# Kernel tuning notes

Hardware: AMD Instinct MI355X
Metric: run time of the kernel (lower is better)

Reference implementation:

```python
import jax, jax.numpy as jnp
import numpy as np

B, S, IN, OUT, R, E = 8, 2048, 4096, 4096, 16, 64
ALPHA = 1.0


def setup_inputs() -> dict:
    ks = jax.random.split(jax.random.key(0), 7)
    return {
        "x": jax.random.normal(ks[0], (B, S, IN), jnp.float32),
        "query_signal": jax.random.normal(ks[1], (B, IN), jnp.float32),
        "A_pool": jax.random.normal(ks[2], (E, R, IN), jnp.float32),
        # original inits B pool to zeros; use small random values for a non-degenerate baseline
        "B_pool": jax.random.normal(ks[3], (E, OUT, R), jnp.float32) * 0.02,
        "W_rA": jax.random.normal(ks[4], (E, IN), jnp.float32) * 0.02,
        "b_rA": jnp.zeros((E,), jnp.float32),
        "W_rB": jax.random.normal(ks[5], (E, IN), jnp.float32) * 0.02,
        "b_rB": jnp.zeros((E,), jnp.float32),
        "cfs_W": jax.random.normal(ks[6], (R, IN, E), jnp.float32),
    }


def reference(x, query_signal, A_pool, B_pool, W_rA, b_rA, W_rB, b_rB, cfs_W):
    ranks = jnp.arange(R)  # rank slot k pairs with the k-th top-k expert index
    # IFS router A -> top-r expert indices per sample
    g_A_scores = query_signal @ W_rA.T + b_rA            # (B, E)
    _, idx_A = jax.lax.top_k(g_A_scores, R)              # (B, R)
    # gather: k-th selected expert contributes its k-th rank row
    lora_A = A_pool[idx_A, ranks[None, :], :]            # (B, R, IN)
    # router B scores: IFS linear + CFS content score (detached lora_A)
    g_B_scores = (query_signal @ W_rB.T + b_rB
                  + jnp.einsum('bri,rie->be', jax.lax.stop_gradient(lora_A), cfs_W))  # (B, E)
    _, idx_B = jax.lax.top_k(g_B_scores, R)              # (B, R)
    lora_B = jnp.transpose(B_pool, (0, 2, 1))[idx_B, ranks[None, :], :]  # (B, R, OUT)
    # two batched low-rank matmuls
    after_A = jnp.einsum('bsi,bri->bsr', x, lora_A)      # (B, S, R)
    lora_delta = jnp.einsum('bsr,bro->bso', after_A, lora_B)  # (B, S, OUT)
    return lora_delta * ALPHA
```

## Files before the change

### kernel.cpp

```cpp
#include <hip/hip_runtime.h>

#define B_ 8
#define S_ 2048
#define IN_ 4096
#define OUT_ 4096
#define R_ 16
#define E_ 64

typedef float v4f __attribute__((ext_vector_type(4)));

__device__ __forceinline__ float4 ntload4(const float* p) {
  v4f t = __builtin_nontemporal_load((const v4f*)p);
  float4 r; r.x = t.x; r.y = t.y; r.z = t.z; r.w = t.w; return r;
}
__device__ __forceinline__ void ntstore4(float* p, float4 v) {
  v4f t; t.x = v.x; t.y = v.y; t.z = v.z; t.w = v.w;
  __builtin_nontemporal_store(t, (v4f*)p);
}

__device__ __forceinline__ float dot4(float4 a, float4 b) {
  return a.x*b.x + a.y*b.y + a.z*b.z + a.w*b.w;
}

__device__ __forceinline__ void topk16(float v, int* __restrict__ dst) {
  const int lane = threadIdx.x & 63;
  for (int r = 0; r < R_; ++r) {
    float mv = v; int mi = lane;
    #pragma unroll
    for (int off = 1; off < 64; off <<= 1) {
      float v2 = __shfl_xor(mv, off, 64);
      int   i2 = __shfl_xor(mi, off, 64);
      if (v2 > mv || (v2 == mv && i2 < mi)) { mv = v2; mi = i2; }
    }
    if (lane == 0) dst[r] = mi;
    if (lane == mi) v = -__builtin_inff();
  }
}

__global__ __launch_bounds__(256) void k_scores(
    const float* __restrict__ q, const float* __restrict__ W_rA,
    const float* __restrict__ b_rA, const float* __restrict__ W_rB,
    const float* __restrict__ b_rB, float* __restrict__ scoresA,
    float* __restrict__ gB0)
{
  const int b = blockIdx.x >> 3, eg = blockIdx.x & 7;
  __shared__ float qs[IN_];
  const int tid = threadIdx.x;
  {
    const float4* q4 = (const float4*)(q + (size_t)b * IN_);
    float4* s4 = (float4*)qs;
    for (int i = tid; i < IN_ / 4; i += 256) s4[i] = q4[i];
  }
  __syncthreads();
  const int wave = tid >> 6, lane = tid & 63;
  const float4* qs4 = (const float4*)qs;
  for (int k = 0; k < 2; ++k) {
    const int e = eg * 8 + wave * 2 + k;
    const float4* wa = (const float4*)(W_rA + (size_t)e * IN_);
    const float4* wb = (const float4*)(W_rB + (size_t)e * IN_);
    float pa = 0.f, pb = 0.f;
    for (int i = lane; i < IN_ / 4; i += 64) {
      float4 qv = qs4[i];
      pa += dot4(qv, wa[i]);
      pb += dot4(qv, wb[i]);
    }
    #pragma unroll
    for (int off = 1; off < 64; off <<= 1) {
      pa += __shfl_xor(pa, off, 64);
      pb += __shfl_xor(pb, off, 64);
    }
    if (lane == 0) {
      scoresA[b * E_ + e] = pa + b_rA[e];
      gB0[b * E_ + e]     = pb + b_rB[e];
    }
  }
}

__global__ __launch_bounds__(64) void k_topk_a(
    const float* __restrict__ scoresA, int* __restrict__ idxA)
{
  const int b = blockIdx.x;
  topk16(scoresA[b * E_ + (threadIdx.x & 63)], idxA + b * R_);
}

__global__ __launch_bounds__(256) void k_cfs(
    const float* __restrict__ A_pool, const float* __restrict__ cfs,
    const int* __restrict__ idxA, float* __restrict__ gBpart)
{
  const int blk = blockIdx.x;
  const int r = blk >> 3, ic = blk & 7;
  __shared__ float as[B_][512];
  __shared__ float red[4][B_][E_];
  const int tid = threadIdx.x;
  {
    const int b = tid >> 5, t = tid & 31;
    const int e = idxA[b * R_ + r];
    const float4* src = (const float4*)(A_pool + ((size_t)e * R_ + r) * IN_ + ic * 512);
    float4* dst = (float4*)as[b];
    for (int j = t; j < 128; j += 32) dst[j] = src[j];
  }
  __syncthreads();
  const int e = tid & 63, part = tid >> 6;
  float acc[B_];
  #pragma unroll
  for (int b = 0; b < B_; ++b) acc[b] = 0.f;
  const float* cbase = cfs + ((size_t)r * IN_ + ic * 512) * E_ + e;
  for (int i = part * 128; i < part * 128 + 128; ++i) {
    float c = __builtin_nontemporal_load(cbase + (size_t)i * E_);
    #pragma unroll
    for (int b = 0; b < B_; ++b) acc[b] += as[b][i] * c;
  }
  #pragma unroll
  for (int b = 0; b < B_; ++b) red[part][b][e] = acc[b];
  __syncthreads();
  if (tid < 64) {
    #pragma unroll
    for (int b = 0; b < B_; ++b)
      gBpart[((size_t)blk * B_ + b) * E_ + tid] =
          red[0][b][tid] + red[1][b][tid] + red[2][b][tid] + red[3][b][tid];
  }
}

__global__ __launch_bounds__(64) void k_topk_b(
    const float* __restrict__ gB0, const float* __restrict__ gBpart,
    int* __restrict__ idxB)
{
  const int b = blockIdx.x;
  const int lane = threadIdx.x & 63;
  float v = gB0[b * E_ + lane];
  for (int blk = 0; blk < 128; ++blk)
    v += gBpart[((size_t)blk * B_ + b) * E_ + lane];
  topk16(v, idxB + b * R_);
}

__global__ __launch_bounds__(256) void k_pack_b(
    const float* __restrict__ B_pool, const int* __restrict__ idxB,
    float* __restrict__ loraBp)
{
  const int bx = blockIdx.x;
  const int b = bx >> 6, r = (bx >> 2) & 15, q = bx & 3;
  const int e = idxB[b * R_ + r];
  const float* src = B_pool + (size_t)e * OUT_ * R_ + r;
  float* dst = loraBp + (size_t)(b * R_ + r) * OUT_;
  #pragma unroll
  for (int i = 0; i < 4; ++i) {
    const int o = q * 1024 + i * 256 + threadIdx.x;
    dst[o] = src[(size_t)o * R_];
  }
}

__global__ __launch_bounds__(256) void k_after(
    const float* __restrict__ x, const float* __restrict__ A_pool,
    const int* __restrict__ idxA, float* __restrict__ partial)
{
  const int bx = blockIdx.x;
  const int rt = bx & 31, b = (bx >> 5) & 7, ks = bx >> 8;
  const int row0 = rt * 64;
  __shared__ float4 As[R_][128];
  __shared__ float aa[64][R_];
  const int tid = threadIdx.x;
  {
    const int sr = tid >> 4, st = tid & 15;
    const float4* src =
        (const float4*)(A_pool + ((size_t)idxA[b * R_ + sr] * R_ + sr) * IN_ + ks * 512);
    #pragma unroll
    for (int j = st; j < 128; j += 16) As[sr][j] = src[j];
  }
  const int rg = tid >> 4, p = tid & 15;
  const float* xbase = x + ((size_t)b * S_ + row0 + rg * 4) * IN_ + ks * 512;
  float acc[4][R_];
  #pragma unroll
  for (int m = 0; m < 4; ++m)
    #pragma unroll
    for (int r = 0; r < R_; ++r) acc[m][r] = 0.f;
  __syncthreads();

  #pragma unroll 2
  for (int step = 0; step < 8; ++step) {
    const int i4 = step * 16 + p;
    float4 xv[4];
    #pragma unroll
    for (int m = 0; m < 4; ++m)
      xv[m] = ntload4(xbase + (size_t)m * IN_ + i4 * 4);
    #pragma unroll
    for (int r = 0; r < R_; ++r) {
      float4 a = As[r][i4];
      #pragma unroll
      for (int m = 0; m < 4; ++m) acc[m][r] += dot4(xv[m], a);
    }
  }
  #pragma unroll
  for (int m = 0; m < 4; ++m)
    #pragma unroll
    for (int r = 0; r < R_; ++r) {
      float v = acc[m][r];
      v += __shfl_xor(v, 1, 64);
      v += __shfl_xor(v, 2, 64);
      v += __shfl_xor(v, 4, 64);
      v += __shfl_xor(v, 8, 64);
      acc[m][r] = v;
    }
  if (p == 0) {
    #pragma unroll
    for (int m = 0; m < 4; ++m) {
      float4* d4 = (float4*)aa[rg * 4 + m];
      d4[0] = make_float4(acc[m][0],  acc[m][1],  acc[m][2],  acc[m][3]);
      d4[1] = make_float4(acc[m][4],  acc[m][5],  acc[m][6],  acc[m][7]);
      d4[2] = make_float4(acc[m][8],  acc[m][9],  acc[m][10], acc[m][11]);
      d4[3] = make_float4(acc[m][12], acc[m][13], acc[m][14], acc[m][15]);
    }
  }
  __syncthreads();
  float4 w = ((const float4*)aa)[tid];
  ntstore4(partial + (((size_t)(b * 32 + rt) * 8 + ks) << 10) + tid * 4, w);
}

__global__ __launch_bounds__(256) void k_out(
    const float* __restrict__ partial, const float* __restrict__ loraBp,
    float* __restrict__ out)
{
  const int bx = blockIdx.x;
  const int b = bx >> 6, st = bx & 63;
  __shared__ float aa[32][R_];
  const int tid = threadIdx.x;
  if (tid < 128) {
    const float* base = partial + (((size_t)(b * 32 + (st >> 1)) * 8) << 10)
                        + (st & 1) * 512 + tid * 4;
    float4 s = ntload4(base);
    #pragma unroll
    for (int k = 1; k < 8; ++k) {
      float4 t = ntload4(base + k * 1024);
      s.x += t.x; s.y += t.y; s.z += t.z; s.w += t.w;
    }
    ((float4*)aa)[tid] = s;
  }
  __syncthreads();
  const int row0 = st * 32;
  for (int oc = 0; oc < 4; ++oc) {
    float4 Bf[R_];
    #pragma unroll
    for (int r = 0; r < R_; ++r)
      Bf[r] = *(const float4*)(loraBp + (size_t)(b * R_ + r) * OUT_ + oc * 1024 + tid * 4);
    float* obase = out + ((size_t)b * S_ + row0) * OUT_ + oc * 1024 + tid * 4;
    #pragma unroll 2
    for (int s = 0; s < 32; ++s) {
      const float4* av = (const float4*)aa[s];
      float4 a0 = av[0], a1 = av[1], a2 = av[2], a3 = av[3];
      float4 o = make_float4(0.f, 0.f, 0.f, 0.f);
      o.x += a0.x*Bf[0].x;  o.y += a0.x*Bf[0].y;  o.z += a0.x*Bf[0].z;  o.w += a0.x*Bf[0].w;
      o.x += a0.y*Bf[1].x;  o.y += a0.y*Bf[1].y;  o.z += a0.y*Bf[1].z;  o.w += a0.y*Bf[1].w;
      o.x += a0.z*Bf[2].x;  o.y += a0.z*Bf[2].y;  o.z += a0.z*Bf[2].z;  o.w += a0.z*Bf[2].w;
      o.x += a0.w*Bf[3].x;  o.y += a0.w*Bf[3].y;  o.z += a0.w*Bf[3].z;  o.w += a0.w*Bf[3].w;
      o.x += a1.x*Bf[4].x;  o.y += a1.x*Bf[4].y;  o.z += a1.x*Bf[4].z;  o.w += a1.x*Bf[4].w;
      o.x += a1.y*Bf[5].x;  o.y += a1.y*Bf[5].y;  o.z += a1.y*Bf[5].z;  o.w += a1.y*Bf[5].w;
      o.x += a1.z*Bf[6].x;  o.y += a1.z*Bf[6].y;  o.z += a1.z*Bf[6].z;  o.w += a1.z*Bf[6].w;
      o.x += a1.w*Bf[7].x;  o.y += a1.w*Bf[7].y;  o.z += a1.w*Bf[7].z;  o.w += a1.w*Bf[7].w;
      o.x += a2.x*Bf[8].x;  o.y += a2.x*Bf[8].y;  o.z += a2.x*Bf[8].z;  o.w += a2.x*Bf[8].w;
      o.x += a2.y*Bf[9].x;  o.y += a2.y*Bf[9].y;  o.z += a2.y*Bf[9].z;  o.w += a2.y*Bf[9].w;
      o.x += a2.z*Bf[10].x; o.y += a2.z*Bf[10].y; o.z += a2.z*Bf[10].z; o.w += a2.z*Bf[10].w;
      o.x += a2.w*Bf[11].x; o.y += a2.w*Bf[11].y; o.z += a2.w*Bf[11].z; o.w += a2.w*Bf[11].w;
      o.x += a3.x*Bf[12].x; o.y += a3.x*Bf[12].y; o.z += a3.x*Bf[12].z; o.w += a3.x*Bf[12].w;
      o.x += a3.y*Bf[13].x; o.y += a3.y*Bf[13].y; o.z += a3.y*Bf[13].z; o.w += a3.y*Bf[13].w;
      o.x += a3.z*Bf[14].x; o.y += a3.z*Bf[14].y; o.z += a3.z*Bf[14].z; o.w += a3.z*Bf[14].w;
      o.x += a3.w*Bf[15].x; o.y += a3.w*Bf[15].y; o.z += a3.w*Bf[15].z; o.w += a3.w*Bf[15].w;
      ntstore4(obase + (size_t)s * OUT_, o);
    }
  }
}

extern "C" void kernel_launch(void* const* d_in, const int* in_sizes, int n_in,
                              void* d_out, int out_size, void* d_ws, size_t ws_size,
                              hipStream_t stream) {
  const float* x      = (const float*)d_in[0];
  const float* qsig   = (const float*)d_in[1];
  const float* A_pool = (const float*)d_in[2];
  const float* B_pool = (const float*)d_in[3];
  const float* W_rA   = (const float*)d_in[4];
  const float* b_rA   = (const float*)d_in[5];
  const float* W_rB   = (const float*)d_in[6];
  const float* b_rB   = (const float*)d_in[7];
  const float* cfs_W  = (const float*)d_in[8];
  float* out = (float*)d_out;

  char* w = (char*)d_ws;
  int*   idxA    = (int*)(w);
  int*   idxB    = (int*)(w + 512);
  float* scoresA = (float*)(w + 1024);
  float* gB0     = (float*)(w + 3072);
  float* gBpart  = (float*)(w + 5120);
  float* loraBp  = (float*)(w + 267264);
  float* partial = (float*)(w + 2364416);

  k_scores<<<64, 256, 0, stream>>>(qsig, W_rA, b_rA, W_rB, b_rB, scoresA, gB0);
  k_topk_a<<<8, 64, 0, stream>>>(scoresA, idxA);
  k_cfs<<<128, 256, 0, stream>>>(A_pool, cfs_W, idxA, gBpart);
  k_topk_b<<<8, 64, 0, stream>>>(gB0, gBpart, idxB);
  k_pack_b<<<512, 256, 0, stream>>>(B_pool, idxB, loraBp);
  k_after<<<2048, 256, 0, stream>>>(x, A_pool, idxA, partial);
  k_out<<<512, 256, 0, stream>>>(partial, loraBp, out);
}
```

Before: 193.5 us.

## Fuse top-k selection into consumer kernels and double output grid

Removes the standalone top-k kernels. Each consumer block (k_cfs, k_after) now recomputes the top-16 of router A scores redundantly into shared memory. The router B top-k is fused with the B-pool packing kernel, which now reduces the CFS partials itself. The output kernel is split into 16-row tiles with twice as many blocks. This cuts kernel launches and serial dependency gaps. In exchange, every block of the 2048-block k_after kernel does redundant top-k work, and each packing block redoes the gBpart reduction.

```diff
diff --git a/kernel.cpp b/kernel.cpp
--- a/kernel.cpp
+++ b/kernel.cpp
@@ -76,25 +76,23 @@
   }
 }
 
-__global__ __launch_bounds__(64) void k_topk_a(
-    const float* __restrict__ scoresA, int* __restrict__ idxA)
-{
-  const int b = blockIdx.x;
-  topk16(scoresA[b * E_ + (threadIdx.x & 63)], idxA + b * R_);
-}
-
 __global__ __launch_bounds__(256) void k_cfs(
     const float* __restrict__ A_pool, const float* __restrict__ cfs,
-    const int* __restrict__ idxA, float* __restrict__ gBpart)
+    const float* __restrict__ scoresA, float* __restrict__ gBpart)
 {
   const int blk = blockIdx.x;
   const int r = blk >> 3, ic = blk & 7;
   __shared__ float as[B_][512];
   __shared__ float red[4][B_][E_];
-  const int tid = threadIdx.x;
+  __shared__ int idxA_s[B_][R_];
+  const int tid = threadIdx.x;
+  const int wave = tid >> 6, lane = tid & 63;
+  for (int bb = wave; bb < B_; bb += 4)
+    topk16(scoresA[bb * E_ + lane], idxA_s[bb]);
+  __syncthreads();
   {
     const int b = tid >> 5, t = tid & 31;
-    const int e = idxA[b * R_ + r];
+    const int e = idxA_s[b][r];
     const float4* src = (const float4*)(A_pool + ((size_t)e * R_ + r) * IN_ + ic * 512);
     float4* dst = (float4*)as[b];
     for (int j = t; j < 128; j += 32) dst[j] = src[j];
@@ -121,48 +119,52 @@
   }
 }
 
-__global__ __launch_bounds__(64) void k_topk_b(
+__global__ __launch_bounds__(256) void k_topkb_pack(
     const float* __restrict__ gB0, const float* __restrict__ gBpart,
-    int* __restrict__ idxB)
-{
-  const int b = blockIdx.x;
-  const int lane = threadIdx.x & 63;
-  float v = gB0[b * E_ + lane];
-  for (int blk = 0; blk < 128; ++blk)
-    v += gBpart[((size_t)blk * B_ + b) * E_ + lane];
-  topk16(v, idxB + b * R_);
-}
-
-__global__ __launch_bounds__(256) void k_pack_b(
-    const float* __restrict__ B_pool, const int* __restrict__ idxB,
-    float* __restrict__ loraBp)
-{
-  const int bx = blockIdx.x;
-  const int b = bx >> 6, r = (bx >> 2) & 15, q = bx & 3;
-  const int e = idxB[b * R_ + r];
+    const float* __restrict__ B_pool, float* __restrict__ loraBp)
+{
+  const int b = blockIdx.x >> 4, r = blockIdx.x & 15;
+  __shared__ float red[4][E_];
+  __shared__ int idxB_s[R_];
+  const int tid = threadIdx.x;
+  const int wave = tid >> 6, lane = tid & 63;
+  float p = 0.f;
+  for (int blk = wave * 32; blk < wave * 32 + 32; ++blk)
+    p += gBpart[((size_t)blk * B_ + b) * E_ + lane];
+  red[wave][lane] = p;
+  __syncthreads();
+  if (wave == 0) {
+    float v = gB0[b * E_ + lane] + red[0][lane] + red[1][lane] + red[2][lane] + red[3][lane];
+    topk16(v, idxB_s);
+  }
+  __syncthreads();
+  const int e = idxB_s[r];
   const float* src = B_pool + (size_t)e * OUT_ * R_ + r;
   float* dst = loraBp + (size_t)(b * R_ + r) * OUT_;
   #pragma unroll
-  for (int i = 0; i < 4; ++i) {
-    const int o = q * 1024 + i * 256 + threadIdx.x;
+  for (int i = 0; i < 16; ++i) {
+    const int o = i * 256 + tid;
     dst[o] = src[(size_t)o * R_];
   }
 }
 
 __global__ __launch_bounds__(256) void k_after(
     const float* __restrict__ x, const float* __restrict__ A_pool,
-    const int* __restrict__ idxA, float* __restrict__ partial)
+    const float* __restrict__ scoresA, float* __restrict__ partial)
 {
   const int bx = blockIdx.x;
   const int rt = bx & 31, b = (bx >> 5) & 7, ks = bx >> 8;
   const int row0 = rt * 64;
   __shared__ float4 As[R_][128];
   __shared__ float aa[64][R_];
-  const int tid = threadIdx.x;
+  __shared__ int idxA_s[R_];
+  const int tid = threadIdx.x;
+  if (tid < 64) topk16(scoresA[b * E_ + tid], idxA_s);
+  __syncthreads();
   {
     const int sr = tid >> 4, st = tid & 15;
     const float4* src =
-        (const float4*)(A_pool + ((size_t)idxA[b * R_ + sr] * R_ + sr) * IN_ + ks * 512);
+        (const float4*)(A_pool + ((size_t)idxA_s[sr] * R_ + sr) * IN_ + ks * 512);
     #pragma unroll
     for (int j = st; j < 128; j += 16) As[sr][j] = src[j];
   }
@@ -220,12 +222,12 @@
     float* __restrict__ out)
 {
   const int bx = blockIdx.x;
-  const int b = bx >> 6, st = bx & 63;
-  __shared__ float aa[32][R_];
-  const int tid = threadIdx.x;
-  if (tid < 128) {
-    const float* base = partial + (((size_t)(b * 32 + (st >> 1)) * 8) << 10)
-                        + (st & 1) * 512 + tid * 4;
+  const int b = bx >> 7, st = bx & 127;
+  __shared__ float aa[16][R_];
+  const int tid = threadIdx.x;
+  if (tid < 64) {
+    const float* base = partial + (((size_t)(b * 32 + (st >> 2)) * 8) << 10)
+                        + (st & 3) * 256 + tid * 4;
     float4 s = ntload4(base);
     #pragma unroll
     for (int k = 1; k < 8; ++k) {
@@ -235,7 +237,8 @@
     ((float4*)aa)[tid] = s;
   }
   __syncthreads();
-  const int row0 = st * 32;
+  const int row0 = st * 16;
+  #pragma unroll
   for (int oc = 0; oc < 4; ++oc) {
     float4 Bf[R_];
     #pragma unroll
@@ -243,7 +246,7 @@
       Bf[r] = *(const float4*)(loraBp + (size_t)(b * R_ + r) * OUT_ + oc * 1024 + tid * 4);
     float* obase = out + ((size_t)b * S_ + row0) * OUT_ + oc * 1024 + tid * 4;
     #pragma unroll 2
-    for (int s = 0; s < 32; ++s) {
+    for (int s = 0; s < 16; ++s) {
       const float4* av = (const float4*)aa[s];
       float4 a0 = av[0], a1 = av[1], a2 = av[2], a3 = av[3];
       float4 o = make_float4(0.f, 0.f, 0.f, 0.f);
@@ -283,19 +286,15 @@
   float* out = (float*)d_out;
 
   char* w = (char*)d_ws;
-  int*   idxA    = (int*)(w);
-  int*   idxB    = (int*)(w + 512);
-  float* scoresA = (float*)(w + 1024);
-  float* gB0     = (float*)(w + 3072);
-  float* gBpart  = (float*)(w + 5120);
-  float* loraBp  = (float*)(w + 267264);
-  float* partial = (float*)(w + 2364416);
+  float* scoresA = (float*)(w);
+  float* gB0     = (float*)(w + 2048);
+  float* gBpart  = (float*)(w + 4096);
+  float* loraBp  = (float*)(w + 266240);
+  float* partial = (float*)(w + 2363392);
 
   k_scores<<<64, 256, 0, stream>>>(qsig, W_rA, b_rA, W_rB, b_rB, scoresA, gB0);
-  k_topk_a<<<8, 64, 0, stream>>>(scoresA, idxA);
-  k_cfs<<<128, 256, 0, stream>>>(A_pool, cfs_W, idxA, gBpart);
-  k_topk_b<<<8, 64, 0, stream>>>(gB0, gBpart, idxB);
-  k_pack_b<<<512, 256, 0, stream>>>(B_pool, idxB, loraBp);
-  k_after<<<2048, 256, 0, stream>>>(x, A_pool, idxA, partial);
-  k_out<<<512, 256, 0, stream>>>(partial, loraBp, out);
-}
+  k_cfs<<<128, 256, 0, stream>>>(A_pool, cfs_W, scoresA, gBpart);
+  k_topkb_pack<<<128, 256, 0, stream>>>(gB0, gBpart, B_pool, loraBp);
+  k_after<<<2048, 256, 0, stream>>>(x, A_pool, scoresA, partial);
+  k_out<<<1024, 256, 0, stream>>>(partial, loraBp, out);
+}
```

Result: slower. 209.6 us (+8.3%).
